# Optimization experiments

Hardware: AMD Instinct MI355X
Metric: run time of the kernel (lower is better)

Reference implementation:

```python
import jax, jax.numpy as jnp
import numpy as np

D, H_DIM, HEADS = 512, 2048, 8

def rmsnorm(x, w):
    eps = jnp.finfo(x.dtype).eps
    return x * jax.lax.rsqrt(jnp.mean(x * x, axis=-1, keepdims=True) + eps) * w

def setup_inputs() -> dict:
    key = jax.random.key(0)
    ks = jax.random.split(key, 16)
    B, N = 2, 2048
    s_d = 1.0 / np.sqrt(D)
    s_h = 1.0 / np.sqrt(H_DIM)
    inp = {
        "x": jax.random.normal(ks[0], (B, N, D), jnp.float32),
        "DA": jax.random.randint(ks[1], (B, 1, N, N), 0, 2, jnp.int32),
        "Wq": jax.random.normal(ks[2], (D, D), jnp.float32) * s_d,
        "bq": jnp.zeros((D,), jnp.float32),
        "Wk": jax.random.normal(ks[3], (D, D), jnp.float32) * s_d,
        "bk": jnp.zeros((D,), jnp.float32),
        "Wv": jax.random.normal(ks[4], (D, D), jnp.float32) * s_d,
        "bv": jnp.zeros((D,), jnp.float32),
        "W1": jax.random.normal(ks[5], (H_DIM, D), jnp.float32) * s_d,
        "b1": jnp.zeros((H_DIM,), jnp.float32),
        "W2": jax.random.normal(ks[6], (H_DIM, D), jnp.float32) * s_d,
        "b2": jnp.zeros((H_DIM,), jnp.float32),
        "W3": jax.random.normal(ks[7], (D, H_DIM), jnp.float32) * s_h,
        "b3": jnp.zeros((D,), jnp.float32),
        "g1": jnp.ones((D,), jnp.float32),
        "g2": jnp.ones((D,), jnp.float32),
    }
    return inp

def reference(x, DA, Wq, bq, Wk, bk, Wv, bv, W1, b1, W2, b2, W3, b3, g1, g2):
    B, N, _ = x.shape
    hd = D // HEADS  # head_dim = 64
    xn = rmsnorm(x, g1)
    # projections (torch Linear: y = x @ W.T + b), split heads -> [B,H,N,hd]
    def split(t):
        return t.reshape(B, N, HEADS, hd).transpose(0, 2, 1, 3)
    q = split(xn @ Wq.T + bq)
    k = split(xn @ Wk.T + bk)
    v = split(xn @ Wv.T + bv)
    scores = jnp.einsum("bhnd,bhmd->bhnm", q, k) / np.sqrt(hd)
    scores = jnp.where(DA == 0, jnp.asarray(-1e20, scores.dtype), scores)
    attn = jax.nn.softmax(scores, axis=-1)
    o = jnp.einsum("bhnm,bhmd->bhnd", attn, v)
    o = o.transpose(0, 2, 1, 3).reshape(B, N, D)
    h = x + o
    hn = rmsnorm(h, g2)
    x2 = hn @ W1.T + b1
    x3 = hn @ W2.T + b2
    out = h + (jax.nn.silu(x2) * x3) @ W3.T + b3
    return out
```

## Files before the change

kernel.cpp:

```cpp
#include <hip/hip_runtime.h>

typedef unsigned short u16;
typedef unsigned int   u32;
typedef unsigned long long u64;

using bf16x8 = __attribute__((ext_vector_type(8))) __bf16;
using f32x4  = __attribute__((ext_vector_type(4))) float;
using us8    = __attribute__((ext_vector_type(8))) u16;
using us4v   = __attribute__((ext_vector_type(4))) u16;

#define NB_TOK   4096
#define DD       512
#define HDIM     2048
#define SEQ      2048
#define EPS_F32  1.1920929e-7f
#define SM_SHIFT 16.0f

__device__ __forceinline__ u16 f32_to_bf16(float f) {
  u32 u = __float_as_uint(f);
  u += 0x7fffu + ((u >> 16) & 1u);
  return (u16)(u >> 16);
}
__device__ __forceinline__ float bf16_to_f32(u16 h) {
  return __uint_as_float(((u32)h) << 16);
}
__device__ __forceinline__ bf16x8 ld_frag(const u16* p) {
  return __builtin_bit_cast(bf16x8, *(const us8*)p);
}
__device__ __forceinline__ void gload_lds16(const void* g, void* l) {
  __builtin_amdgcn_global_load_lds(
      (__attribute__((address_space(1))) void*)(void*)g,
      (__attribute__((address_space(3))) void*)l, 16, 0, 0);
}

__global__ __launch_bounds__(256) void k_pre(
    const float* __restrict__ wq, const float* __restrict__ wk,
    const float* __restrict__ wv, const float* __restrict__ w1,
    const float* __restrict__ w2, const float* __restrict__ w3,
    const int* __restrict__ da, const float* __restrict__ x,
    const float* __restrict__ g1,
    u16* __restrict__ wqkv, u16* __restrict__ w1b,
    u16* __restrict__ w2b, u16* __restrict__ w3b,
    u64* __restrict__ maskT, u16* __restrict__ xn) {
  int bx = blockIdx.x;
  if (bx < 3840) {
    int e = (bx * 256 + threadIdx.x) * 4;
    const float* src; u16* dst; int off;
    if      (e <  262144) { src = wq; dst = wqkv;          off = e; }
    else if (e <  524288) { src = wk; dst = wqkv + 262144; off = e -  262144; }
    else if (e <  786432) { src = wv; dst = wqkv + 524288; off = e -  524288; }
    else if (e < 1835008) { src = w1; dst = w1b;           off = e -  786432; }
    else if (e < 2883584) { src = w2; dst = w2b;           off = e - 1835008; }
    else                  { src = w3; dst = w3b;           off = e - 2883584; }
    float4 v = *(const float4*)(src + off);
    us4v o;
    o[0] = f32_to_bf16(v.x); o[1] = f32_to_bf16(v.y);
    o[2] = f32_to_bf16(v.z); o[3] = f32_to_bf16(v.w);
    *(us4v*)(dst + off) = o;
  } else if (bx < 4864) {
    int lane = threadIdx.x & 63, wave = threadIdx.x >> 6;
    int row = (bx - 3840) * 4 + wave;
    int b = row >> 11, r = row & 2047;
    const int* src = da + (size_t)row * SEQ;
    #pragma unroll 4
    for (int w = 0; w < 32; ++w) {
      int d = src[w * 64 + lane];
      u64 bal = __ballot(d != 0);
      if (lane == 0) maskT[((size_t)(b * 32 + w)) * SEQ + r] = bal;
    }
  } else {
    int lane = threadIdx.x & 63, wave = threadIdx.x >> 6;
    int row = (bx - 4864) * 4 + wave;
    size_t base = (size_t)row * DD + lane * 8;
    float4 a = *(const float4*)(x + base);
    float4 b = *(const float4*)(x + base + 4);
    float ss = a.x*a.x + a.y*a.y + a.z*a.z + a.w*a.w
             + b.x*b.x + b.y*b.y + b.z*b.z + b.w*b.w;
    #pragma unroll
    for (int m = 1; m < 64; m <<= 1) ss += __shfl_xor(ss, m);
    float sc = rsqrtf(ss * (1.0f / DD) + EPS_F32);
    float4 ga = *(const float4*)(g1 + lane * 8);
    float4 gb = *(const float4*)(g1 + lane * 8 + 4);
    us8 o;
    o[0] = f32_to_bf16(a.x * sc * ga.x); o[1] = f32_to_bf16(a.y * sc * ga.y);
    o[2] = f32_to_bf16(a.z * sc * ga.z); o[3] = f32_to_bf16(a.w * sc * ga.w);
    o[4] = f32_to_bf16(b.x * sc * gb.x); o[5] = f32_to_bf16(b.y * sc * gb.y);
    o[6] = f32_to_bf16(b.z * sc * gb.z); o[7] = f32_to_bf16(b.w * sc * gb.w);
    *(us8*)(xn + base) = o;
  }
}

template <int NB>
__device__ __forceinline__ void gemm64(const u16* __restrict__ A,
                                       const u16* __restrict__ B0,
                                       const u16* __restrict__ B1,
                                       int K, int mblk, int nblk,
                                       int kbeg, int kend,
                                       u16* lA, u16* lB,
                                       f32x4 (*acc)[4][4]) {
  const int tid = threadIdx.x, lane = tid & 63, wave = tid >> 6;
  const int l15 = lane & 15, quad = lane >> 4;
  const int wmt = (wave >> 1) * 4, wnt = (wave & 1) * 4;
  for (int k0 = kbeg; k0 < kend; k0 += 64) {
    #pragma unroll
    for (int i = 0; i < 4; ++i) {
      int c = wave * 4 + i;
      int mt = c >> 1, ks = c & 1;
      size_t gofs = (size_t)(mt * 16 + l15) * K + k0 + ks * 32 + quad * 8;
      gload_lds16(A + (size_t)mblk * K + gofs, lA + c * 512);
      gload_lds16(B0 + (size_t)nblk * K + gofs, lB + c * 512);
      if constexpr (NB == 2)
        gload_lds16(B1 + (size_t)nblk * K + gofs, lB + 8192 + c * 512);
    }
    __syncthreads();
    #pragma unroll
    for (int ks = 0; ks < 2; ++ks) {
      bf16x8 af[4];
      #pragma unroll
      for (int mt = 0; mt < 4; ++mt)
        af[mt] = ld_frag(lA + (wmt + mt) * 1024 + ks * 512 + lane * 8);
      #pragma unroll
      for (int bi = 0; bi < NB; ++bi)
        #pragma unroll
        for (int nt = 0; nt < 4; ++nt) {
          bf16x8 b = ld_frag(lB + bi * 8192 + (wnt + nt) * 1024 + ks * 512 + lane * 8);
          #pragma unroll
          for (int mt = 0; mt < 4; ++mt)
            acc[bi][mt][nt] = __builtin_amdgcn_mfma_f32_16x16x32_bf16(
                af[mt], b, acc[bi][mt][nt], 0, 0, 0);
        }
    }
    __syncthreads();
  }
}

__global__ __launch_bounds__(256) void k_qkv(const u16* __restrict__ xn,
                                             const u16* __restrict__ wqkv,
                                             const float* __restrict__ bq,
                                             const float* __restrict__ bk,
                                             const float* __restrict__ bv,
                                             u16* __restrict__ qb,
                                             u16* __restrict__ kb,
                                             u16* __restrict__ vt) {
  __shared__ u16 lA[8192], lB[8192];
  int z = blockIdx.z;
  const u16* Bp = wqkv + z * (DD * DD);
  const float* bias = (z == 0) ? bq : ((z == 1) ? bk : bv);
  float scale = (z == 0) ? 0.125f : 1.0f;
  int mblk = blockIdx.x * 128, nblk = blockIdx.y * 128;
  f32x4 acc[1][4][4];
  #pragma unroll
  for (int mt = 0; mt < 4; ++mt)
    #pragma unroll
    for (int nt = 0; nt < 4; ++nt) acc[0][mt][nt] = (f32x4)0.0f;
  gemm64<1>(xn, Bp, nullptr, DD, mblk, nblk, 0, DD, lA, lB, acc);
  int lane = threadIdx.x & 63, wave = threadIdx.x >> 6;
  int l15 = lane & 15, quad = lane >> 4;
  int wm = (wave >> 1) * 64, wn = (wave & 1) * 64;
  if (z < 2) {
    u16* out = z ? kb : qb;
    #pragma unroll
    for (int mt = 0; mt < 4; ++mt)
      #pragma unroll
      for (int nt = 0; nt < 4; ++nt) {
        int n = nblk + wn + nt * 16 + l15;
        float bn = bias[n];
        #pragma unroll
        for (int r = 0; r < 4; ++r) {
          int m = mblk + wm + mt * 16 + quad * 4 + r;
          out[(size_t)m * DD + n] = f32_to_bf16((acc[0][mt][nt][r] + bn) * scale);
        }
      }
  } else {
    #pragma unroll
    for (int mt = 0; mt < 4; ++mt)
      #pragma unroll
      for (int nt = 0; nt < 4; ++nt) {
        int n = nblk + wn + nt * 16 + l15;
        float bn = bias[n];
        int m = mblk + wm + mt * 16 + quad * 4;
        int b = m >> 11, tok = m & 2047;
        us4v o;
        #pragma unroll
        for (int r = 0; r < 4; ++r) o[r] = f32_to_bf16(acc[0][mt][nt][r] + bn);
        *(us4v*)(vt + ((size_t)(b * 8 + (n >> 6)) * 64 + (n & 63)) * SEQ + tok) = o;
      }
  }
}

__global__ __launch_bounds__(256) void k_attn(const u16* __restrict__ q,
                                              const u16* __restrict__ k,
                                              const u16* __restrict__ vT,
                                              const u64* __restrict__ maskT,
                                              u16* __restrict__ Opart,
                                              float* __restrict__ lpart) {
  __shared__ u16 lQ[8192], lK[8192], lV[8192], lP[4 * 32 * 72];
  int tid = threadIdx.x, lane = tid & 63, wave = tid >> 6;
  int l15 = lane & 15, quad = lane >> 4;
  int bh = blockIdx.y, b = bh >> 3, h = bh & 7;
  int q0 = blockIdx.x * 128;
  int z = blockIdx.z;
  int kvbase = z * 1024;
  const u16* qg = q + (size_t)(b * SEQ + q0) * DD + h * 64;
  const u16* kg = k + (size_t)(b * SEQ + kvbase) * DD + h * 64;
  const u16* vg = vT + (size_t)bh * 64 * SEQ + kvbase;
  const u64* mg = maskT + ((size_t)(b * 32 + z * 16)) * SEQ + q0 + wave * 32 + l15;

  #pragma unroll
  for (int i = 0; i < 4; ++i) {
    int c = wave * 4 + i;
    int nt = c >> 1, ks = c & 1;
    gload_lds16(qg + (size_t)(nt * 16 + l15) * DD + ks * 32 + quad * 8, lQ + c * 512);
  }
  #pragma unroll
  for (int i = 0; i < 2; ++i) {
    int c = wave * 2 + i;
    int mt = c >> 1, ks = c & 1;
    gload_lds16(kg + (size_t)(mt * 16 + l15) * DD + ks * 32 + quad * 8, lK + c * 512);
    gload_lds16(vg + (size_t)(mt * 16 + l15) * SEQ + ks * 32 + quad * 8, lV + c * 512);
  }
  __syncthreads();

  bf16x8 qa[2][2];
  #pragma unroll
  for (int nq = 0; nq < 2; ++nq)
    #pragma unroll
    for (int ks = 0; ks < 2; ++ks)
      qa[nq][ks] = ld_frag(lQ + (wave * 2 + nq) * 1024 + ks * 512 + lane * 8);

  f32x4 oa[2][4];
  float ls[2] = {0.0f, 0.0f};
  #pragma unroll
  for (int mq = 0; mq < 2; ++mq)
    #pragma unroll
    for (int dt = 0; dt < 4; ++dt) oa[mq][dt] = (f32x4)0.0f;

  u16* pw = lP + wave * 2304;

  for (int t = 0; t < 16; ++t) {
    const u16* lKc = lK + (t & 1) * 4096;
    const u16* lVc = lV + (t & 1) * 4096;

    u64 mw[2];
    #pragma unroll
    for (int nq = 0; nq < 2; ++nq)
      mw[nq] = mg[(size_t)t * SEQ + nq * 16] >> (quad * 4);

    if (t + 1 < 16) {
      int kv1 = (t + 1) * 64;
      u16* dK = lK + ((t + 1) & 1) * 4096;
      u16* dV = lV + ((t + 1) & 1) * 4096;
      #pragma unroll
      for (int i = 0; i < 2; ++i) {
        int c = wave * 2 + i;
        int mt = c >> 1, ks = c & 1;
        gload_lds16(kg + (size_t)(kv1 + mt * 16 + l15) * DD + ks * 32 + quad * 8, dK + c * 512);
        gload_lds16(vg + (size_t)(mt * 16 + l15) * SEQ + kv1 + ks * 32 + quad * 8, dV + c * 512);
      }
    }

    f32x4 sa[2][4];
    #pragma unroll
    for (int nq = 0; nq < 2; ++nq)
      #pragma unroll
      for (int mt = 0; mt < 4; ++mt) sa[nq][mt] = (f32x4)0.0f;
    #pragma unroll
    for (int ks = 0; ks < 2; ++ks) {
      bf16x8 ka[4];
      #pragma unroll
      for (int mt = 0; mt < 4; ++mt)
        ka[mt] = ld_frag(lKc + mt * 1024 + ks * 512 + lane * 8);
      #pragma unroll
      for (int nq = 0; nq < 2; ++nq)
        #pragma unroll
        for (int mt = 0; mt < 4; ++mt)
          sa[nq][mt] = __builtin_amdgcn_mfma_f32_16x16x32_bf16(
              ka[mt], qa[nq][ks], sa[nq][mt], 0, 0, 0);
    }

    #pragma unroll
    for (int nq = 0; nq < 2; ++nq)
      #pragma unroll
      for (int mt = 0; mt < 4; ++mt) {
        u32 nib = (u32)(mw[nq] >> (mt * 16)) & 0xFu;
        u32 pb[4];
        #pragma unroll
        for (int r = 0; r < 4; ++r) {
          float p = __expf(sa[nq][mt][r] - SM_SHIFT);
          p = (nib >> r) & 1u ? p : 0.0f;
          u32 ub = __float_as_uint(p) & 0xffff0000u;
          ls[nq] += __uint_as_float(ub);
          pb[r] = ub;
        }
        u32 lo = __builtin_amdgcn_perm(pb[1], pb[0], 0x07060302u);
        u32 hi = __builtin_amdgcn_perm(pb[3], pb[2], 0x07060302u);
        u64 pk = ((u64)hi << 32) | lo;
        *(u64*)(pw + (nq * 16 + l15) * 72 + mt * 16 + quad * 4) = pk;
      }

    #pragma unroll
    for (int ks = 0; ks < 2; ++ks) {
      bf16x8 pa[2], vb[4];
      #pragma unroll
      for (int mq = 0; mq < 2; ++mq)
        pa[mq] = ld_frag(pw + (mq * 16 + l15) * 72 + ks * 32 + quad * 8);
      #pragma unroll
      for (int dt = 0; dt < 4; ++dt)
        vb[dt] = ld_frag(lVc + dt * 1024 + ks * 512 + lane * 8);
      #pragma unroll
      for (int mq = 0; mq < 2; ++mq)
        #pragma unroll
        for (int dt = 0; dt < 4; ++dt)
          oa[mq][dt] = __builtin_amdgcn_mfma_f32_16x16x32_bf16(
              pa[mq], vb[dt], oa[mq][dt], 0, 0, 0);
    }

    __syncthreads();
  }

  #pragma unroll
  for (int nq = 0; nq < 2; ++nq) {
    ls[nq] += __shfl_xor(ls[nq], 16);
    ls[nq] += __shfl_xor(ls[nq], 32);
    if (quad == 0)
      lpart[((size_t)z * 16 + bh) * SEQ + q0 + wave * 32 + nq * 16 + l15] = ls[nq];
  }

  u16* Og = Opart + (size_t)z * NB_TOK * DD;
  #pragma unroll
  for (int mq = 0; mq < 2; ++mq)
    #pragma unroll
    for (int r = 0; r < 4; ++r) {
      int m = q0 + wave * 32 + mq * 16 + quad * 4 + r;
      u16* dst = Og + (size_t)(b * SEQ + m) * DD + h * 64;
      #pragma unroll
      for (int dt = 0; dt < 4; ++dt)
        dst[dt * 16 + l15] = f32_to_bf16(oa[mq][dt][r]);
    }
}

__global__ __launch_bounds__(256) void k_rms2(const float* __restrict__ x,
                                              const u16* __restrict__ Opart,
                                              const float* __restrict__ lpart,
                                              const float* __restrict__ b3,
                                              const float* __restrict__ g2,
                                              float* __restrict__ outinit,
                                              u16* __restrict__ hn) {
  int lane = threadIdx.x & 63, wave = threadIdx.x >> 6;
  int row = blockIdx.x * 4 + wave;
  int b = row >> 11, tok = row & 2047, hh = lane >> 3;
  size_t base = (size_t)row * DD + lane * 8;
  float l0 = lpart[(size_t)(b * 8 + hh) * SEQ + tok];
  float l1 = lpart[(size_t)(16 + b * 8 + hh) * SEQ + tok];
  float lsum = l0 + l1;
  float inv = (lsum > 0.0f) ? (1.0f / lsum) : 0.0f;
  float4 a = *(const float4*)(x + base);
  float4 bb = *(const float4*)(x + base + 4);
  us8 o0 = *(const us8*)(Opart + base);
  us8 o1 = *(const us8*)(Opart + (size_t)NB_TOK * DD + base);
  float hv[8];
  hv[0] = a.x  + (bf16_to_f32(o0[0]) + bf16_to_f32(o1[0])) * inv;
  hv[1] = a.y  + (bf16_to_f32(o0[1]) + bf16_to_f32(o1[1])) * inv;
  hv[2] = a.z  + (bf16_to_f32(o0[2]) + bf16_to_f32(o1[2])) * inv;
  hv[3] = a.w  + (bf16_to_f32(o0[3]) + bf16_to_f32(o1[3])) * inv;
  hv[4] = bb.x + (bf16_to_f32(o0[4]) + bf16_to_f32(o1[4])) * inv;
  hv[5] = bb.y + (bf16_to_f32(o0[5]) + bf16_to_f32(o1[5])) * inv;
  hv[6] = bb.z + (bf16_to_f32(o0[6]) + bf16_to_f32(o1[6])) * inv;
  hv[7] = bb.w + (bf16_to_f32(o0[7]) + bf16_to_f32(o1[7])) * inv;
  float ss = 0.0f;
  #pragma unroll
  for (int j = 0; j < 8; ++j) ss += hv[j] * hv[j];
  #pragma unroll
  for (int m = 1; m < 64; m <<= 1) ss += __shfl_xor(ss, m);
  float sc = rsqrtf(ss * (1.0f / DD) + EPS_F32);
  float4 c0 = *(const float4*)(b3 + lane * 8);
  float4 c1 = *(const float4*)(b3 + lane * 8 + 4);
  float4 w0 = {hv[0] + c0.x, hv[1] + c0.y, hv[2] + c0.z, hv[3] + c0.w};
  float4 w1 = {hv[4] + c1.x, hv[5] + c1.y, hv[6] + c1.z, hv[7] + c1.w};
  *(float4*)(outinit + base) = w0;
  *(float4*)(outinit + base + 4) = w1;
  float4 ga = *(const float4*)(g2 + lane * 8);
  float4 gb = *(const float4*)(g2 + lane * 8 + 4);
  us8 hb;
  hb[0] = f32_to_bf16(hv[0] * sc * ga.x); hb[1] = f32_to_bf16(hv[1] * sc * ga.y);
  hb[2] = f32_to_bf16(hv[2] * sc * ga.z); hb[3] = f32_to_bf16(hv[3] * sc * ga.w);
  hb[4] = f32_to_bf16(hv[4] * sc * gb.x); hb[5] = f32_to_bf16(hv[5] * sc * gb.y);
  hb[6] = f32_to_bf16(hv[6] * sc * gb.z); hb[7] = f32_to_bf16(hv[7] * sc * gb.w);
  *(us8*)(hn + base) = hb;
}

__global__ __launch_bounds__(256) void k_ffn12(const u16* __restrict__ hn,
                                               const u16* __restrict__ w1,
                                               const u16* __restrict__ w2,
                                               const float* __restrict__ b1,
                                               const float* __restrict__ b2,
                                               u16* __restrict__ g) {
  __shared__ u16 lA[8192], lB[16384];
  int mblk = blockIdx.x * 128, nblk = blockIdx.y * 128;
  f32x4 acc[2][4][4];
  #pragma unroll
  for (int bi = 0; bi < 2; ++bi)
    #pragma unroll
    for (int mt = 0; mt < 4; ++mt)
      #pragma unroll
      for (int nt = 0; nt < 4; ++nt) acc[bi][mt][nt] = (f32x4)0.0f;
  gemm64<2>(hn, w1, w2, DD, mblk, nblk, 0, DD, lA, lB, acc);
  int lane = threadIdx.x & 63, wave = threadIdx.x >> 6;
  int l15 = lane & 15, quad = lane >> 4;
  int wm = (wave >> 1) * 64, wn = (wave & 1) * 64;
  #pragma unroll
  for (int mt = 0; mt < 4; ++mt)
    #pragma unroll
    for (int nt = 0; nt < 4; ++nt) {
      int n = nblk + wn + nt * 16 + l15;
      float bb1 = b1[n], bb2 = b2[n];
      #pragma unroll
      for (int r = 0; r < 4; ++r) {
        int m = mblk + wm + mt * 16 + quad * 4 + r;
        float x2 = acc[0][mt][nt][r] + bb1;
        float x3 = acc[1][mt][nt][r] + bb2;
        float si = x2 / (1.0f + __expf(-x2));
        g[(size_t)m * HDIM + n] = f32_to_bf16(si * x3);
      }
    }
}

__global__ __launch_bounds__(256) void k_ffn3(const u16* __restrict__ g,
                                              const u16* __restrict__ w3,
                                              float* __restrict__ out) {
  __shared__ u16 lA[8192], lB[8192];
  int mblk = blockIdx.x * 128, nblk = blockIdx.y * 128, z = blockIdx.z;
  f32x4 acc[1][4][4];
  #pragma unroll
  for (int mt = 0; mt < 4; ++mt)
    #pragma unroll
    for (int nt = 0; nt < 4; ++nt) acc[0][mt][nt] = (f32x4)0.0f;
  gemm64<1>(g, w3, nullptr, HDIM, mblk, nblk, z * 512, z * 512 + 512, lA, lB, acc);
  int lane = threadIdx.x & 63, wave = threadIdx.x >> 6;
  int l15 = lane & 15, quad = lane >> 4;
  int wm = (wave >> 1) * 64, wn = (wave & 1) * 64;
  #pragma unroll
  for (int mt = 0; mt < 4; ++mt)
    #pragma unroll
    for (int nt = 0; nt < 4; ++nt) {
      int n = nblk + wn + nt * 16 + l15;
      #pragma unroll
      for (int r = 0; r < 4; ++r) {
        int m = mblk + wm + mt * 16 + quad * 4 + r;
        atomicAdd(out + (size_t)m * DD + n, acc[0][mt][nt][r]);
      }
    }
}

#define MB(x) ((size_t)(x) * 1048576)
#define WS_XN    MB(0)
#define WS_WQKV  MB(4)
#define WS_W1B   MB(6)
#define WS_W2B   MB(8)
#define WS_W3B   MB(10)
#define WS_MASK  MB(12)
#define WS_QB    MB(16)
#define WS_KB    MB(20)
#define WS_VT    MB(24)
#define WS_OP    MB(28)
#define WS_LP    MB(44)
#define WS_HN    MB(45)
#define WS_G     MB(49)

extern "C" void kernel_launch(void* const* d_in, const int* in_sizes, int n_in,
                              void* d_out, int out_size, void* d_ws, size_t ws_size,
                              hipStream_t stream) {
  (void)in_sizes; (void)n_in; (void)out_size; (void)ws_size;
  const float* x  = (const float*)d_in[0];
  const int*   DA = (const int*)d_in[1];
  const float* Wq = (const float*)d_in[2];
  const float* bq = (const float*)d_in[3];
  const float* Wk = (const float*)d_in[4];
  const float* bk = (const float*)d_in[5];
  const float* Wv = (const float*)d_in[6];
  const float* bv = (const float*)d_in[7];
  const float* W1 = (const float*)d_in[8];
  const float* b1 = (const float*)d_in[9];
  const float* W2 = (const float*)d_in[10];
  const float* b2 = (const float*)d_in[11];
  const float* W3 = (const float*)d_in[12];
  const float* b3 = (const float*)d_in[13];
  const float* g1 = (const float*)d_in[14];
  const float* g2 = (const float*)d_in[15];
  float* out = (float*)d_out;
  char* w = (char*)d_ws;

  u16* xn   = (u16*)(w + WS_XN);
  u16* wqkv = (u16*)(w + WS_WQKV);
  u16* w1b  = (u16*)(w + WS_W1B);
  u16* w2b  = (u16*)(w + WS_W2B);
  u16* w3b  = (u16*)(w + WS_W3B);
  u64* mskT = (u64*)(w + WS_MASK);
  u16* qb   = (u16*)(w + WS_QB);
  u16* kb   = (u16*)(w + WS_KB);
  u16* vt   = (u16*)(w + WS_VT);
  u16* Op   = (u16*)(w + WS_OP);
  float* lp = (float*)(w + WS_LP);
  u16* hn   = (u16*)(w + WS_HN);
  u16* gb   = (u16*)(w + WS_G);

  k_pre<<<5888, 256, 0, stream>>>(Wq, Wk, Wv, W1, W2, W3, DA, x, g1,
                                  wqkv, w1b, w2b, w3b, mskT, xn);
  k_qkv<<<dim3(32, 4, 3), 256, 0, stream>>>(xn, wqkv, bq, bk, bv, qb, kb, vt);
  k_attn<<<dim3(16, 16, 2), 256, 0, stream>>>(qb, kb, vt, mskT, Op, lp);
  k_rms2<<<1024, 256, 0, stream>>>(x, Op, lp, b3, g2, out, hn);
  k_ffn12<<<dim3(32, 16), 256, 0, stream>>>(hn, w1b, w2b, b1, b2, gb);
  k_ffn3<<<dim3(32, 4, 4), 256, 0, stream>>>(gb, w3b, out);
}
```

Before: 288.2 us.

## Shrink GEMM tiles, double-buffer K loop, split attention KV four ways

Replaces the 128x128 GEMM helper with a 128x64-tile version. It steps through K in chunks of 32 using two LDS buffers, so the next chunk loads while MFMAs run on the current one. The QKV, FFN12 and FFN3 grids double and get a launch-bounds occupancy hint. Attention now splits the KV range into four parts instead of two, and the residual/RMSNorm kernel sums four partial outputs and normalisers. The aim is more blocks to fill the CUs and hidden load latency, at the cost of more partial-result traffic and lower per-block data reuse.

```diff
diff --git a/kernel.cpp b/kernel.cpp
--- a/kernel.cpp
+++ b/kernel.cpp
@@ -91,78 +91,86 @@
 }
 
 template <int NB>
-__device__ __forceinline__ void gemm64(const u16* __restrict__ A,
+__device__ __forceinline__ void gemm32(const u16* __restrict__ A,
                                        const u16* __restrict__ B0,
                                        const u16* __restrict__ B1,
                                        int K, int mblk, int nblk,
-                                       int kbeg, int kend,
+                                       int kbeg, int iters,
                                        u16* lA, u16* lB,
-                                       f32x4 (*acc)[4][4]) {
-  const int tid = threadIdx.x, lane = tid & 63, wave = tid >> 6;
+                                       f32x4 (*acc)[4][2]) {
+  const int lane = threadIdx.x & 63, wave = threadIdx.x >> 6;
   const int l15 = lane & 15, quad = lane >> 4;
-  const int wmt = (wave >> 1) * 4, wnt = (wave & 1) * 4;
-  for (int k0 = kbeg; k0 < kend; k0 += 64) {
-    #pragma unroll
-    for (int i = 0; i < 4; ++i) {
-      int c = wave * 4 + i;
-      int mt = c >> 1, ks = c & 1;
-      size_t gofs = (size_t)(mt * 16 + l15) * K + k0 + ks * 32 + quad * 8;
-      gload_lds16(A + (size_t)mblk * K + gofs, lA + c * 512);
-      gload_lds16(B0 + (size_t)nblk * K + gofs, lB + c * 512);
-      if constexpr (NB == 2)
-        gload_lds16(B1 + (size_t)nblk * K + gofs, lB + 8192 + c * 512);
-    }
+  const int wmt = (wave >> 1) * 4, wnt = (wave & 1) * 2;
+  constexpr int CPW = 2 + NB;
+
+  auto stage = [&](int buf, int k0) {
+    #pragma unroll
+    for (int i = 0; i < CPW; ++i) {
+      int id = wave * CPW + i;
+      if (id < 8) {
+        gload_lds16(A + (size_t)(mblk + id * 16 + l15) * K + k0 + quad * 8,
+                    lA + buf * 4096 + id * 512);
+      } else {
+        int id2 = id - 8, bi = id2 >> 2, nt = id2 & 3;
+        const u16* B = bi ? B1 : B0;
+        gload_lds16(B + (size_t)(nblk + nt * 16 + l15) * K + k0 + quad * 8,
+                    lB + bi * 4096 + buf * 2048 + nt * 512);
+      }
+    }
+  };
+
+  stage(0, kbeg);
+  __syncthreads();
+  for (int it = 0; it < iters; ++it) {
+    if (it + 1 < iters) stage((it + 1) & 1, kbeg + (it + 1) * 32);
+    int buf = it & 1;
+    bf16x8 af[4];
+    #pragma unroll
+    for (int mt = 0; mt < 4; ++mt)
+      af[mt] = ld_frag(lA + buf * 4096 + (wmt + mt) * 512 + lane * 8);
+    #pragma unroll
+    for (int bi = 0; bi < NB; ++bi)
+      #pragma unroll
+      for (int nt = 0; nt < 2; ++nt) {
+        bf16x8 b = ld_frag(lB + bi * 4096 + buf * 2048 + (wnt + nt) * 512 + lane * 8);
+        #pragma unroll
+        for (int mt = 0; mt < 4; ++mt)
+          acc[bi][mt][nt] = __builtin_amdgcn_mfma_f32_16x16x32_bf16(
+              af[mt], b, acc[bi][mt][nt], 0, 0, 0);
+      }
     __syncthreads();
-    #pragma unroll
-    for (int ks = 0; ks < 2; ++ks) {
-      bf16x8 af[4];
-      #pragma unroll
-      for (int mt = 0; mt < 4; ++mt)
-        af[mt] = ld_frag(lA + (wmt + mt) * 1024 + ks * 512 + lane * 8);
-      #pragma unroll
-      for (int bi = 0; bi < NB; ++bi)
-        #pragma unroll
-        for (int nt = 0; nt < 4; ++nt) {
-          bf16x8 b = ld_frag(lB + bi * 8192 + (wnt + nt) * 1024 + ks * 512 + lane * 8);
-          #pragma unroll
-          for (int mt = 0; mt < 4; ++mt)
-            acc[bi][mt][nt] = __builtin_amdgcn_mfma_f32_16x16x32_bf16(
-                af[mt], b, acc[bi][mt][nt], 0, 0, 0);
-        }
-    }
-    __syncthreads();
-  }
-}
-
-__global__ __launch_bounds__(256) void k_qkv(const u16* __restrict__ xn,
-                                             const u16* __restrict__ wqkv,
-                                             const float* __restrict__ bq,
-                                             const float* __restrict__ bk,
-                                             const float* __restrict__ bv,
-                                             u16* __restrict__ qb,
-                                             u16* __restrict__ kb,
-                                             u16* __restrict__ vt) {
-  __shared__ u16 lA[8192], lB[8192];
+  }
+}
+
+__global__ __launch_bounds__(256, 4) void k_qkv(const u16* __restrict__ xn,
+                                                const u16* __restrict__ wqkv,
+                                                const float* __restrict__ bq,
+                                                const float* __restrict__ bk,
+                                                const float* __restrict__ bv,
+                                                u16* __restrict__ qb,
+                                                u16* __restrict__ kb,
+                                                u16* __restrict__ vt) {
+  __shared__ u16 lA[8192], lB[4096];
   int z = blockIdx.z;
   const u16* Bp = wqkv + z * (DD * DD);
   const float* bias = (z == 0) ? bq : ((z == 1) ? bk : bv);
   float scale = (z == 0) ? 0.125f : 1.0f;
-  int mblk = blockIdx.x * 128, nblk = blockIdx.y * 128;
-  f32x4 acc[1][4][4];
+  int mblk = blockIdx.x * 128, nblk = blockIdx.y * 64;
+  f32x4 acc[1][4][2];
   #pragma unroll
   for (int mt = 0; mt < 4; ++mt)
     #pragma unroll
-    for (int nt = 0; nt < 4; ++nt) acc[0][mt][nt] = (f32x4)0.0f;
-  gemm64<1>(xn, Bp, nullptr, DD, mblk, nblk, 0, DD, lA, lB, acc);
+    for (int nt = 0; nt < 2; ++nt) acc[0][mt][nt] = (f32x4)0.0f;
+  gemm32<1>(xn, Bp, nullptr, DD, mblk, nblk, 0, 16, lA, lB, acc);
   int lane = threadIdx.x & 63, wave = threadIdx.x >> 6;
   int l15 = lane & 15, quad = lane >> 4;
-  int wm = (wave >> 1) * 64, wn = (wave & 1) * 64;
+  int wm = (wave >> 1) * 64, wn = (wave & 1) * 32;
   if (z < 2) {
     u16* out = z ? kb : qb;
     #pragma unroll
     for (int mt = 0; mt < 4; ++mt)
       #pragma unroll
-      for (int nt = 0; nt < 4; ++nt) {
+      for (int nt = 0; nt < 2; ++nt) {
         int n = nblk + wn + nt * 16 + l15;
         float bn = bias[n];
         #pragma unroll
@@ -175,7 +183,7 @@
     #pragma unroll
     for (int mt = 0; mt < 4; ++mt)
       #pragma unroll
-      for (int nt = 0; nt < 4; ++nt) {
+      for (int nt = 0; nt < 2; ++nt) {
         int n = nblk + wn + nt * 16 + l15;
         float bn = bias[n];
         int m = mblk + wm + mt * 16 + quad * 4;
@@ -200,11 +208,11 @@
   int bh = blockIdx.y, b = bh >> 3, h = bh & 7;
   int q0 = blockIdx.x * 128;
   int z = blockIdx.z;
-  int kvbase = z * 1024;
+  int kvbase = z * 512;
   const u16* qg = q + (size_t)(b * SEQ + q0) * DD + h * 64;
   const u16* kg = k + (size_t)(b * SEQ + kvbase) * DD + h * 64;
   const u16* vg = vT + (size_t)bh * 64 * SEQ + kvbase;
-  const u64* mg = maskT + ((size_t)(b * 32 + z * 16)) * SEQ + q0 + wave * 32 + l15;
+  const u64* mg = maskT + ((size_t)(b * 32 + z * 8)) * SEQ + q0 + wave * 32 + l15;
 
   #pragma unroll
   for (int i = 0; i < 4; ++i) {
@@ -237,7 +245,7 @@
 
   u16* pw = lP + wave * 2304;
 
-  for (int t = 0; t < 16; ++t) {
+  for (int t = 0; t < 8; ++t) {
     const u16* lKc = lK + (t & 1) * 4096;
     const u16* lVc = lV + (t & 1) * 4096;
 
@@ -246,7 +254,7 @@
     for (int nq = 0; nq < 2; ++nq)
       mw[nq] = mg[(size_t)t * SEQ + nq * 16] >> (quad * 4);
 
-    if (t + 1 < 16) {
+    if (t + 1 < 8) {
       int kv1 = (t + 1) * 64;
       u16* dK = lK + ((t + 1) & 1) * 4096;
       u16* dV = lV + ((t + 1) & 1) * 4096;
@@ -350,23 +358,25 @@
   int row = blockIdx.x * 4 + wave;
   int b = row >> 11, tok = row & 2047, hh = lane >> 3;
   size_t base = (size_t)row * DD + lane * 8;
-  float l0 = lpart[(size_t)(b * 8 + hh) * SEQ + tok];
-  float l1 = lpart[(size_t)(16 + b * 8 + hh) * SEQ + tok];
-  float lsum = l0 + l1;
+  float lsum = 0.0f;
+  #pragma unroll
+  for (int z = 0; z < 4; ++z)
+    lsum += lpart[((size_t)(z * 16 + b * 8 + hh)) * SEQ + tok];
   float inv = (lsum > 0.0f) ? (1.0f / lsum) : 0.0f;
+  float ov[8] = {0,0,0,0,0,0,0,0};
+  #pragma unroll
+  for (int z = 0; z < 4; ++z) {
+    us8 o = *(const us8*)(Opart + (size_t)z * NB_TOK * DD + base);
+    #pragma unroll
+    for (int j = 0; j < 8; ++j) ov[j] += bf16_to_f32(o[j]);
+  }
   float4 a = *(const float4*)(x + base);
   float4 bb = *(const float4*)(x + base + 4);
-  us8 o0 = *(const us8*)(Opart + base);
-  us8 o1 = *(const us8*)(Opart + (size_t)NB_TOK * DD + base);
   float hv[8];
-  hv[0] = a.x  + (bf16_to_f32(o0[0]) + bf16_to_f32(o1[0])) * inv;
-  hv[1] = a.y  + (bf16_to_f32(o0[1]) + bf16_to_f32(o1[1])) * inv;
-  hv[2] = a.z  + (bf16_to_f32(o0[2]) + bf16_to_f32(o1[2])) * inv;
-  hv[3] = a.w  + (bf16_to_f32(o0[3]) + bf16_to_f32(o1[3])) * inv;
-  hv[4] = bb.x + (bf16_to_f32(o0[4]) + bf16_to_f32(o1[4])) * inv;
-  hv[5] = bb.y + (bf16_to_f32(o0[5]) + bf16_to_f32(o1[5])) * inv;
-  hv[6] = bb.z + (bf16_to_f32(o0[6]) + bf16_to_f32(o1[6])) * inv;
-  hv[7] = bb.w + (bf16_to_f32(o0[7]) + bf16_to_f32(o1[7])) * inv;
+  hv[0] = a.x  + ov[0] * inv; hv[1] = a.y  + ov[1] * inv;
+  hv[2] = a.z  + ov[2] * inv; hv[3] = a.w  + ov[3] * inv;
+  hv[4] = bb.x + ov[4] * inv; hv[5] = bb.y + ov[5] * inv;
+  hv[6] = bb.z + ov[6] * inv; hv[7] = bb.w + ov[7] * inv;
   float ss = 0.0f;
   #pragma unroll
   for (int j = 0; j < 8; ++j) ss += hv[j] * hv[j];
@@ -389,29 +399,29 @@
   *(us8*)(hn + base) = hb;
 }
 
-__global__ __launch_bounds__(256) void k_ffn12(const u16* __restrict__ hn,
-                                               const u16* __restrict__ w1,
-                                               const u16* __restrict__ w2,
-                                               const float* __restrict__ b1,
-                                               const float* __restrict__ b2,
-                                               u16* __restrict__ g) {
-  __shared__ u16 lA[8192], lB[16384];
-  int mblk = blockIdx.x * 128, nblk = blockIdx.y * 128;
-  f32x4 acc[2][4][4];
+__global__ __launch_bounds__(256, 4) void k_ffn12(const u16* __restrict__ hn,
+                                                  const u16* __restrict__ w1,
+                                                  const u16* __restrict__ w2,
+                                                  const float* __restrict__ b1,
+                                                  const float* __restrict__ b2,
+                                                  u16* __restrict__ g) {
+  __shared__ u16 lA[8192], lB[8192];
+  int mblk = blockIdx.x * 128, nblk = blockIdx.y * 64;
+  f32x4 acc[2][4][2];
   #pragma unroll
   for (int bi = 0; bi < 2; ++bi)
     #pragma unroll
     for (int mt = 0; mt < 4; ++mt)
       #pragma unroll
-      for (int nt = 0; nt < 4; ++nt) acc[bi][mt][nt] = (f32x4)0.0f;
-  gemm64<2>(hn, w1, w2, DD, mblk, nblk, 0, DD, lA, lB, acc);
+      for (int nt = 0; nt < 2; ++nt) acc[bi][mt][nt] = (f32x4)0.0f;
+  gemm32<2>(hn, w1, w2, DD, mblk, nblk, 0, 16, lA, lB, acc);
   int lane = threadIdx.x & 63, wave = threadIdx.x >> 6;
   int l15 = lane & 15, quad = lane >> 4;
-  int wm = (wave >> 1) * 64, wn = (wave & 1) * 64;
+  int wm = (wave >> 1) * 64, wn = (wave & 1) * 32;
   #pragma unroll
   for (int mt = 0; mt < 4; ++mt)
     #pragma unroll
-    for (int nt = 0; nt < 4; ++nt) {
+    for (int nt = 0; nt < 2; ++nt) {
       int n = nblk + wn + nt * 16 + l15;
       float bb1 = b1[n], bb2 = b2[n];
       #pragma unroll
@@ -425,24 +435,24 @@
     }
 }
 
-__global__ __launch_bounds__(256) void k_ffn3(const u16* __restrict__ g,
-                                              const u16* __restrict__ w3,
-                                              float* __restrict__ out) {
-  __shared__ u16 lA[8192], lB[8192];
-  int mblk = blockIdx.x * 128, nblk = blockIdx.y * 128, z = blockIdx.z;
-  f32x4 acc[1][4][4];
+__global__ __launch_bounds__(256, 4) void k_ffn3(const u16* __restrict__ g,
+                                                 const u16* __restrict__ w3,
+                                                 float* __restrict__ out) {
+  __shared__ u16 lA[8192], lB[4096];
+  int mblk = blockIdx.x * 128, nblk = blockIdx.y * 64, z = blockIdx.z;
+  f32x4 acc[1][4][2];
   #pragma unroll
   for (int mt = 0; mt < 4; ++mt)
     #pragma unroll
-    for (int nt = 0; nt < 4; ++nt) acc[0][mt][nt] = (f32x4)0.0f;
-  gemm64<1>(g, w3, nullptr, HDIM, mblk, nblk, z * 512, z * 512 + 512, lA, lB, acc);
+    for (int nt = 0; nt < 2; ++nt) acc[0][mt][nt] = (f32x4)0.0f;
+  gemm32<1>(g, w3, nullptr, HDIM, mblk, nblk, z * 512, 16, lA, lB, acc);
   int lane = threadIdx.x & 63, wave = threadIdx.x >> 6;
   int l15 = lane & 15, quad = lane >> 4;
-  int wm = (wave >> 1) * 64, wn = (wave & 1) * 64;
+  int wm = (wave >> 1) * 64, wn = (wave & 1) * 32;
   #pragma unroll
   for (int mt = 0; mt < 4; ++mt)
     #pragma unroll
-    for (int nt = 0; nt < 4; ++nt) {
+    for (int nt = 0; nt < 2; ++nt) {
       int n = nblk + wn + nt * 16 + l15;
       #pragma unroll
       for (int r = 0; r < 4; ++r) {
@@ -506,9 +516,9 @@
 
   k_pre<<<5888, 256, 0, stream>>>(Wq, Wk, Wv, W1, W2, W3, DA, x, g1,
                                   wqkv, w1b, w2b, w3b, mskT, xn);
-  k_qkv<<<dim3(32, 4, 3), 256, 0, stream>>>(xn, wqkv, bq, bk, bv, qb, kb, vt);
-  k_attn<<<dim3(16, 16, 2), 256, 0, stream>>>(qb, kb, vt, mskT, Op, lp);
+  k_qkv<<<dim3(32, 8, 3), 256, 0, stream>>>(xn, wqkv, bq, bk, bv, qb, kb, vt);
+  k_attn<<<dim3(16, 16, 4), 256, 0, stream>>>(qb, kb, vt, mskT, Op, lp);
   k_rms2<<<1024, 256, 0, stream>>>(x, Op, lp, b3, g2, out, hn);
-  k_ffn12<<<dim3(32, 16), 256, 0, stream>>>(hn, w1b, w2b, b1, b2, gb);
-  k_ffn3<<<dim3(32, 4, 4), 256, 0, stream>>>(gb, w3b, out);
-}
+  k_ffn12<<<dim3(32, 32), 256, 0, stream>>>(hn, w1b, w2b, b1, b2, gb);
+  k_ffn3<<<dim3(32, 8, 4), 256, 0, stream>>>(gb, w3b, out);
+}
```

Result: no change. 283.7 us (-1.5%).
